# Kernel tuning notes

Hardware: AMD Instinct MI355X
Metric: run time of the kernel (lower is better)

The kernel has to match this reference:

```python
import jax, jax.numpy as jnp
import numpy as np

B, N, C = 1, 2048, 2048
H, KV, D = 32, 8, 64          # query heads, kv heads, head_dim
G = H // KV                    # groups per kv head
EPS = 1e-6
ROPE_BASE = 10000.0


def rmsnorm(x, w, eps=EPS):
    # normalize over the full last dim (H*D or KV*D), as in the module
    var = jnp.mean(jnp.square(x), axis=-1, keepdims=True)
    return x * jax.lax.rsqrt(var + eps) * w


def rope(x):
    # x: [B, N, h, D]; interleaved-pair rotary embedding (torchtune style)
    b, n, h, d = x.shape
    half = d // 2
    inv_freq = 1.0 / (ROPE_BASE ** (jnp.arange(0, d, 2, dtype=jnp.float32) / d))  # [half]
    ang = jnp.arange(n, dtype=jnp.float32)[:, None] * inv_freq[None, :]           # [N, half]
    cos = jnp.cos(ang)[None, :, None, :]
    sin = jnp.sin(ang)[None, :, None, :]
    xr = x.reshape(b, n, h, half, 2)
    x1, x2 = xr[..., 0], xr[..., 1]
    out = jnp.stack([x1 * cos - x2 * sin, x1 * sin + x2 * cos], axis=-1)
    return out.reshape(b, n, h, d)


def setup_inputs() -> dict:
    key = jax.random.key(0)
    ks = jax.random.split(key, 7)
    s = 0.02
    return {
        "x": jax.random.normal(ks[0], (B, N, C), dtype=jnp.float32),
        "wq": jax.random.normal(ks[1], (H * D, C), dtype=jnp.float32) * s,
        "wk": jax.random.normal(ks[2], (KV * D, C), dtype=jnp.float32) * s,
        "wv": jax.random.normal(ks[3], (KV * D, C), dtype=jnp.float32) * s,
        "wo": jax.random.normal(ks[4], (C, C), dtype=jnp.float32) * s,
        "q_norm_w": 1.0 + 0.01 * jax.random.normal(ks[5], (H * D,), dtype=jnp.float32),
        "k_norm_w": 1.0 + 0.01 * jax.random.normal(ks[6], (KV * D,), dtype=jnp.float32),
    }


def reference(x, wq, wk, wv, wo, q_norm_w, k_norm_w):
    scale = D ** -0.5
    q = jnp.einsum("bnc,oc->bno", x, wq)   # [B,N,H*D]
    k = jnp.einsum("bnc,oc->bno", x, wk)   # [B,N,KV*D]
    v = jnp.einsum("bnc,oc->bno", x, wv)
    q = rmsnorm(q, q_norm_w)               # QK-RMSNorm over flat head dims
    k = rmsnorm(k, k_norm_w)
    q = rope(q.reshape(B, N, H, D))
    k = rope(k.reshape(B, N, KV, D))
    v = v.reshape(B, N, KV, D)
    # GQA: group query heads per kv head, no explicit k/v expand
    qg = q.reshape(B, N, KV, G, D)
    scores = jnp.einsum("bnkgd,bmkd->bkgnm", qg, k) * scale  # [B,KV,G,N,N]
    causal = jnp.tril(jnp.ones((N, N), dtype=bool))
    scores = jnp.where(causal[None, None, None], scores, jnp.finfo(scores.dtype).min)
    probs = jax.nn.softmax(scores, axis=-1)
    out = jnp.einsum("bkgnm,bmkd->bnkgd", probs, v).reshape(B, N, H * D)
    return jnp.einsum("bno,co->bnc", out, wo)
```

## Files before the change

### kernel.cpp

```cpp
#include <hip/hip_runtime.h>

typedef __attribute__((ext_vector_type(8))) short short8;
typedef __attribute__((ext_vector_type(4))) float f32x4;

#define MFMA_BF16 __builtin_amdgcn_mfma_f32_16x16x32_bf16

__device__ __forceinline__ unsigned short f2bf(float f) {
  unsigned u = __builtin_bit_cast(unsigned, f);
  u += 0x7fffu + ((u >> 16) & 1u);
  return (unsigned short)(u >> 16);
}

__device__ __forceinline__ unsigned cvtpk(float a, float b) {
  unsigned r;
  asm("v_cvt_pk_bf16_f32 %0, %1, %2" : "=v"(r) : "v"(a), "v"(b));
  return r;
}

__global__ __launch_bounds__(256) void f2b5_kernel(const float* __restrict__ x,
                                                   const float* __restrict__ wq,
                                                   const float* __restrict__ wk,
                                                   const float* __restrict__ wv,
                                                   const float* __restrict__ wo,
                                                   unsigned short* __restrict__ xb,
                                                   unsigned short* __restrict__ wb,
                                                   unsigned short* __restrict__ wob) {
  const int b = blockIdx.x;
  const float* src;
  unsigned short* dst;
  int base;
  if (b < 4096)      { src = x;  dst = xb;                base = b; }
  else if (b < 8192) { src = wq; dst = wb;                base = b - 4096; }
  else if (b < 9216) { src = wk; dst = wb + 2048 * 2048;  base = b - 8192; }
  else if (b < 10240){ src = wv; dst = wb + 2560 * 2048;  base = b - 9216; }
  else               { src = wo; dst = wob;               base = b - 10240; }
  const int i = base * 256 + threadIdx.x;
  const float4 v = ((const float4*)src)[i];
  ushort4 o = make_ushort4(f2bf(v.x), f2bf(v.y), f2bf(v.z), f2bf(v.w));
  ((ushort4*)dst)[i] = o;
}

__global__ __launch_bounds__(256) void trig_kernel(float* __restrict__ cosT, float* __restrict__ sinT) {
  int i = blockIdx.x * 256 + threadIdx.x;
  int n = i >> 5, f = i & 31;
  double ang = (double)n * pow(10000.0, -(double)f / 32.0);
  cosT[i] = (float)cos(ang);
  sinT[i] = (float)sin(ang);
}

__global__ __launch_bounds__(256) void add2_kernel(const float* __restrict__ a,
                                                   const float* __restrict__ b,
                                                   float* __restrict__ o) {
  int i = blockIdx.x * 256 + threadIdx.x;
#pragma unroll
  for (int s = 0; s < 2; ++s) {
    const float4 u = ((const float4*)a)[i], v = ((const float4*)b)[i];
    ((float4*)o)[i] = make_float4(u.x + v.x, u.y + v.y, u.z + v.z, u.w + v.w);
    i += 524288;
  }
}

__global__ __launch_bounds__(256) void gemm_bt(const short* __restrict__ A,
                                               const short* __restrict__ B,
                                               float* __restrict__ C,
                                               int M, int N, int K, int KC) {
  __shared__ __align__(16) short As[2][128 * 32];
  __shared__ __align__(16) short Bs[2][128 * 32];
  const int tid = threadIdx.x;
  const int w = tid >> 6, lane = tid & 63;
  const int fr = lane & 15, fs = lane >> 4;
  const size_t brow = (size_t)blockIdx.y * 128, bcol = (size_t)blockIdx.x * 128;
  const int wr = (w >> 1) * 64, wc = (w & 1) * 64;
  const int lr = tid >> 2;
  const int lcS = ((tid & 3) ^ (lr & 3)) * 8;
  const int ks = blockIdx.z * KC;
  C += (size_t)blockIdx.z * ((size_t)M * N);
  const short* ga = A + (brow + lr) * (size_t)K + lcS + ks;
  const short* gb = B + (bcol + lr) * (size_t)K + lcS + ks;
  f32x4 acc[4][4] = {};

  auto stage = [&](int sb, int k0) {
    short* lA = As[sb] + w * 512;
    short* lB = Bs[sb] + w * 512;
    __builtin_amdgcn_global_load_lds((__attribute__((address_space(1))) void*)(ga + k0),
                                     (__attribute__((address_space(3))) void*)(lA), 16, 0, 0);
    __builtin_amdgcn_global_load_lds((__attribute__((address_space(1))) void*)(ga + (size_t)64 * K + k0),
                                     (__attribute__((address_space(3))) void*)(lA + 2048), 16, 0, 0);
    __builtin_amdgcn_global_load_lds((__attribute__((address_space(1))) void*)(gb + k0),
                                     (__attribute__((address_space(3))) void*)(lB), 16, 0, 0);
    __builtin_amdgcn_global_load_lds((__attribute__((address_space(1))) void*)(gb + (size_t)64 * K + k0),
                                     (__attribute__((address_space(3))) void*)(lB + 2048), 16, 0, 0);
  };

  const int nk = KC >> 5;
  stage(0, 0);
  __syncthreads();
  int buf = 0;
  for (int t = 0; t < nk; ++t) {
    if (t + 1 < nk) stage(buf ^ 1, (t + 1) * 32);
    short8 af[4], bfr[4];
#pragma unroll
    for (int m = 0; m < 4; ++m)
      af[m] = *(const short8*)(As[buf] + (wr + m * 16 + fr) * 32 + ((fs ^ (fr & 3)) * 8));
#pragma unroll
    for (int n = 0; n < 4; ++n)
      bfr[n] = *(const short8*)(Bs[buf] + (wc + n * 16 + fr) * 32 + ((fs ^ (fr & 3)) * 8));
#pragma unroll
    for (int m = 0; m < 4; ++m)
#pragma unroll
      for (int n = 0; n < 4; ++n)
        acc[m][n] = MFMA_BF16(af[m], bfr[n], acc[m][n], 0, 0, 0);
    __syncthreads();
    buf ^= 1;
  }
#pragma unroll
  for (int m = 0; m < 4; ++m)
#pragma unroll
    for (int n = 0; n < 4; ++n)
#pragma unroll
      for (int j = 0; j < 4; ++j)
        C[(brow + wr + m * 16 + fs * 4 + j) * (size_t)N + bcol + wc + n * 16 + fr] = acc[m][n][j];
}

__global__ __launch_bounds__(256) void prep_kernel(const float* __restrict__ qkv,
                                                   const float* __restrict__ qw,
                                                   const float* __restrict__ kw,
                                                   const float* __restrict__ cosT,
                                                   const float* __restrict__ sinT,
                                                   short* __restrict__ qb,
                                                   short* __restrict__ kb,
                                                   short* __restrict__ vbt) {
  const int n = blockIdx.x, t = threadIdx.x;
  const int w = t >> 6, lane = t & 63;
  __shared__ float redq[4], redk[4];
  const float* rowA = qkv + (size_t)n * 3072;
  const float* rowB = rowA + 6291456;
  const float* cT = cosT + n * 32;
  const float* sT = sinT + n * 32;
  const float4* r4a = (const float4*)rowA;
  const float4* r4b = (const float4*)rowB;
  float4 a0 = r4a[t * 2], a1 = r4b[t * 2];
  float4 b0 = r4a[t * 2 + 1], b1 = r4b[t * 2 + 1];
  float4 a = make_float4(a0.x + a1.x, a0.y + a1.y, a0.z + a1.z, a0.w + a1.w);
  float4 b = make_float4(b0.x + b1.x, b0.y + b1.y, b0.z + b1.z, b0.w + b1.w);
  float ss = a.x*a.x + a.y*a.y + a.z*a.z + a.w*a.w + b.x*b.x + b.y*b.y + b.z*b.z + b.w*b.w;
#pragma unroll
  for (int off = 32; off > 0; off >>= 1) ss += __shfl_xor(ss, off);
  if (lane == 0) redq[w] = ss;
  __syncthreads();
  float rsq = rsqrtf((redq[0] + redq[1] + redq[2] + redq[3]) * (1.0f / 2048.f) + 1e-6f)
              * 0.125f * 1.44269504088896f;
  const int base = t * 8;
  float y[8] = {a.x, a.y, a.z, a.w, b.x, b.y, b.z, b.w};
#pragma unroll
  for (int e = 0; e < 8; ++e) y[e] *= rsq * qw[base + e];
  short8 ov;
  const int dbase = base & 63;
#pragma unroll
  for (int p = 0; p < 4; ++p) {
    float c = cT[(dbase >> 1) + p], s = sT[(dbase >> 1) + p];
    float x1 = y[2 * p], x2 = y[2 * p + 1];
    ov[2 * p]     = (short)f2bf(x1 * c - x2 * s);
    ov[2 * p + 1] = (short)f2bf(x1 * s + x2 * c);
  }
  const int h = base >> 6;
  *(short8*)(qb + ((size_t)h * 2048 + n) * 64 + dbase) = ov;
  const int ki = t * 2;
  float2 k0 = *(const float2*)(rowA + 2048 + ki);
  float2 k1 = *(const float2*)(rowB + 2048 + ki);
  float2 kv2 = make_float2(k0.x + k1.x, k0.y + k1.y);
  float ssk = kv2.x * kv2.x + kv2.y * kv2.y;
#pragma unroll
  for (int off = 32; off > 0; off >>= 1) ssk += __shfl_xor(ssk, off);
  if (lane == 0) redk[w] = ssk;
  __syncthreads();
  float rsk = rsqrtf((redk[0] + redk[1] + redk[2] + redk[3]) * (1.0f / 512.f) + 1e-6f);
  float z0 = kv2.x * rsk * kw[ki], z1 = kv2.y * rsk * kw[ki + 1];
  const int kd = ki & 63, kvh = ki >> 6;
  {
    float c = cT[kd >> 1], s = sT[kd >> 1];
    ushort2 o2 = make_ushort2(f2bf(z0 * c - z1 * s), f2bf(z0 * s + z1 * c));
    *(ushort2*)(kb + ((size_t)kvh * 2048 + n) * 64 + kd) = o2;
  }
  float2 v0 = *(const float2*)(rowA + 2560 + ki);
  float2 v1 = *(const float2*)(rowB + 2560 + ki);
  vbt[((size_t)kvh * 64 + kd) * 2048 + n]       = (short)f2bf(v0.x + v1.x);
  vbt[((size_t)kvh * 64 + kd + 1) * 2048 + n]   = (short)f2bf(v0.y + v1.y);
}

__global__ __launch_bounds__(256, 4) void attn_kernel(const short* __restrict__ qb,
                                                      const short* __restrict__ kb,
                                                      const short* __restrict__ vbt,
                                                      short* __restrict__ ab) {
  const int bid = blockIdx.x;
  const int h = bid & 31;
  const int qblk = 31 - (bid >> 5);
  const int kvh = h >> 2;
  const int tid = threadIdx.x;
  const int w = tid >> 6, lane = tid & 63;
  const int fr = lane & 15, fs = lane >> 4;
  const int q0w = qblk * 64 + w * 16;
  const int q_lane = q0w + fr;
  __shared__ __align__(16) short Ks[2][64][64];
  __shared__ __align__(16) short Vs[2][64][64];
  __shared__ __align__(16) short Ps[4][16][64];
  const short* Kb = kb + (size_t)kvh * 2048 * 64;
  const short* Vb = vbt + (size_t)kvh * 64 * 2048;
  short8 qf[2];
  {
    const short* qrow = qb + ((size_t)h * 2048 + q_lane) * 64;
    qf[0] = *(const short8*)(qrow + fs * 8);
    qf[1] = *(const short8*)(qrow + 32 + fs * 8);
  }
  short8 ones8;
#pragma unroll
  for (int e = 0; e < 8; ++e) ones8[e] = (short)0x3F80;
  f32x4 accO[4] = {};
  f32x4 lacc = {};
  float m = -1e30f;
  short* prow = &Ps[w][fr][0];
  const int swz = (fr & 7) << 1;

  const int rS = lane >> 3;
  const int cS = (lane & 7) ^ rS;
  auto stage = [&](int sb, int kv0s) {
#pragma unroll
    for (int i = 0; i < 2; ++i) {
      int r = i * 32 + w * 8 + rS;
      __builtin_amdgcn_global_load_lds(
          (__attribute__((address_space(1))) void*)(Kb + (size_t)(kv0s + r) * 64 + cS * 8),
          (__attribute__((address_space(3))) void*)(&Ks[sb][0][0] + i * 2048 + w * 512), 16, 0, 0);
      __builtin_amdgcn_global_load_lds(
          (__attribute__((address_space(1))) void*)(Vb + (size_t)r * 2048 + kv0s + cS * 8),
          (__attribute__((address_space(3))) void*)(&Vs[sb][0][0] + i * 2048 + w * 512), 16, 0, 0);
    }
  };

  const int ntiles = qblk + 1;
  int buf = 0;
  stage(0, 0);
  __syncthreads();
  for (int t = 0; t < ntiles; ++t) {
    const int kv0 = t * 64;
    if (t + 1 < ntiles) stage(buf ^ 1, (t + 1) * 64);
    const short* KsB = &Ks[buf][0][0];
    const short* VsB = &Vs[buf][0][0];
    const int sw = (fr & 7);
    f32x4 sc[4];
#pragma unroll
    for (int ct = 0; ct < 4; ++ct) {
      const int rk = ct * 16 + fr;
      short8 kf0 = *(const short8*)(KsB + rk * 64 + ((fs ^ sw) * 8));
      short8 kf1 = *(const short8*)(KsB + rk * 64 + (((4 + fs) ^ sw) * 8));
      f32x4 a = {};
      a = MFMA_BF16(kf0, qf[0], a, 0, 0, 0);
      a = MFMA_BF16(kf1, qf[1], a, 0, 0, 0);
      sc[ct] = a;
    }
    if (t == qblk) {
#pragma unroll
      for (int ct = 0; ct < 4; ++ct) {
        const int kvb = kv0 + ct * 16 + fs * 4;
#pragma unroll
        for (int j = 0; j < 4; ++j)
          if (kvb + j > q_lane) sc[ct][j] = -1e30f;
      }
    }
    float v0m = fmaxf(fmaxf(sc[0][0], sc[0][1]), fmaxf(sc[0][2], sc[0][3]));
    float v1m = fmaxf(fmaxf(sc[1][0], sc[1][1]), fmaxf(sc[1][2], sc[1][3]));
    float v2m = fmaxf(fmaxf(sc[2][0], sc[2][1]), fmaxf(sc[2][2], sc[2][3]));
    float v3m = fmaxf(fmaxf(sc[3][0], sc[3][1]), fmaxf(sc[3][2], sc[3][3]));
    float vmax = fmaxf(fmaxf(v0m, v1m), fmaxf(v2m, v3m));
    vmax = fmaxf(vmax, __shfl_xor(vmax, 16));
    vmax = fmaxf(vmax, __shfl_xor(vmax, 32));
    if (!__all(vmax - m <= 8.0f)) {
      float mn = fmaxf(m, vmax);
      float resc = exp2f(m - mn);
      m = mn;
      lacc *= resc;
#pragma unroll
      for (int dt = 0; dt < 4; ++dt)
#pragma unroll
        for (int j = 0; j < 4; ++j) accO[dt][j] *= resc;
    }
#pragma unroll
    for (int ct = 0; ct < 4; ++ct) {
      uint2 pk;
      pk.x = cvtpk(exp2f(sc[ct][0] - m), exp2f(sc[ct][1] - m));
      pk.y = cvtpk(exp2f(sc[ct][2] - m), exp2f(sc[ct][3] - m));
      *(uint2*)(prow + (((ct * 4 + fs) ^ swz) * 4)) = pk;
    }
    short8 pa[2];
#pragma unroll
    for (int s = 0; s < 2; ++s)
      pa[s] = *(const short8*)(prow + (((s * 8 + fs * 2) ^ swz) * 4));
    __builtin_amdgcn_s_setprio(1);
    lacc = MFMA_BF16(ones8, pa[0], lacc, 0, 0, 0);
    lacc = MFMA_BF16(ones8, pa[1], lacc, 0, 0, 0);
#pragma unroll
    for (int dt = 0; dt < 4; ++dt) {
      const int rv = dt * 16 + fr;
      short8 vf0 = *(const short8*)(VsB + rv * 64 + ((fs ^ sw) * 8));
      short8 vf1 = *(const short8*)(VsB + rv * 64 + (((4 + fs) ^ sw) * 8));
      accO[dt] = MFMA_BF16(vf0, pa[0], accO[dt], 0, 0, 0);
      accO[dt] = MFMA_BF16(vf1, pa[1], accO[dt], 0, 0, 0);
    }
    __builtin_amdgcn_s_setprio(0);
    __syncthreads();
    buf ^= 1;
  }
  const float inv = 1.0f / lacc[0];
  short* orow = ab + (size_t)q_lane * 2048 + h * 64;
#pragma unroll
  for (int dt = 0; dt < 4; ++dt) {
    uint2 o;
    o.x = cvtpk(accO[dt][0] * inv, accO[dt][1] * inv);
    o.y = cvtpk(accO[dt][2] * inv, accO[dt][3] * inv);
    *(uint2*)(orow + dt * 16 + fs * 4) = o;
  }
}

extern "C" void kernel_launch(void* const* d_in, const int* in_sizes, int n_in,
                              void* d_out, int out_size, void* d_ws, size_t ws_size,
                              hipStream_t stream) {
  const float* x  = (const float*)d_in[0];
  const float* wq = (const float*)d_in[1];
  const float* wk = (const float*)d_in[2];
  const float* wv = (const float*)d_in[3];
  const float* wo = (const float*)d_in[4];
  const float* qw = (const float*)d_in[5];
  const float* kw = (const float*)d_in[6];
  float* out = (float*)d_out;
  char* ws = (char*)d_ws;
  short* xb    = (short*)(ws + 0);
  short* wb    = (short*)(ws + 8388608);
  short* wob   = (short*)(ws + 20971520);
  float* qkvfA = (float*)(ws + 29360128);
  float* qkvfB = (float*)(ws + 54525952);
  short* qb    = (short*)(ws + 79691776);
  short* kb    = (short*)(ws + 88080384);
  short* vbt   = (short*)(ws + 90177536);
  float* cosT  = (float*)(ws + 92274688);
  float* sinT  = (float*)(ws + 92536832);
  short* ab = xb;
  float* po0 = qkvfA;
  float* po1 = qkvfA + 4194304;
  (void)qkvfB; (void)ws_size;

  f2b5_kernel<<<14336, 256, 0, stream>>>(x, wq, wk, wv, wo,
                                         (unsigned short*)xb, (unsigned short*)wb,
                                         (unsigned short*)wob);
  trig_kernel<<<256, 256, 0, stream>>>(cosT, sinT);
  gemm_bt<<<dim3(24, 16, 2), 256, 0, stream>>>(xb, wb, qkvfA, 2048, 3072, 2048, 1024);
  prep_kernel<<<2048, 256, 0, stream>>>(qkvfA, qw, kw, cosT, sinT, qb, kb, vbt);
  attn_kernel<<<1024, 256, 0, stream>>>(qb, kb, vbt, ab);
  gemm_bt<<<dim3(16, 16, 2), 256, 0, stream>>>(ab, wob, po0, 2048, 2048, 2048, 1024);
  add2_kernel<<<2048, 256, 0, stream>>>(po0, po1, out);
}
```

Baseline: 155.0 us.

## Process 128 query rows per attention block with two 16-row tiles per wave

The attention kernel now gives each wave 32 query rows (two 16-row MFMA tiles), so every block covers 128 queries and the grid halves to 512 blocks. Each K/V tile staged in LDS is reused across twice as many queries, which cuts global-to-LDS traffic and staging overhead per unit of work. Block order is changed to pair heavy and light causal blocks, and waves skip KV tiles that lie entirely above their rows. In exchange, register pressure roughly doubles (occupancy hint drops from 4 to 2), there are fewer blocks to spread over the CUs, and waves inside a block finish their causal work unevenly.

```diff
diff --git a/kernel.cpp b/kernel.cpp
--- a/kernel.cpp
+++ b/kernel.cpp
@@ -188,37 +188,37 @@
   vbt[((size_t)kvh * 64 + kd + 1) * 2048 + n]   = (short)f2bf(v0.y + v1.y);
 }
 
-__global__ __launch_bounds__(256, 4) void attn_kernel(const short* __restrict__ qb,
+__global__ __launch_bounds__(256, 2) void attn_kernel(const short* __restrict__ qb,
                                                       const short* __restrict__ kb,
                                                       const short* __restrict__ vbt,
                                                       short* __restrict__ ab) {
   const int bid = blockIdx.x;
   const int h = bid & 31;
-  const int qblk = 31 - (bid >> 5);
+  const int idx = bid >> 5;
+  const int qblk = idx < 8 ? 15 - idx : idx - 8;
   const int kvh = h >> 2;
   const int tid = threadIdx.x;
   const int w = tid >> 6, lane = tid & 63;
   const int fr = lane & 15, fs = lane >> 4;
-  const int q0w = qblk * 64 + w * 16;
-  const int q_lane = q0w + fr;
+  const int q0w = qblk * 128 + w * 32;
   __shared__ __align__(16) short Ks[2][64][64];
   __shared__ __align__(16) short Vs[2][64][64];
-  __shared__ __align__(16) short Ps[4][16][64];
+  __shared__ __align__(16) short Ps[4][2][16][64];
   const short* Kb = kb + (size_t)kvh * 2048 * 64;
   const short* Vb = vbt + (size_t)kvh * 64 * 2048;
-  short8 qf[2];
-  {
-    const short* qrow = qb + ((size_t)h * 2048 + q_lane) * 64;
-    qf[0] = *(const short8*)(qrow + fs * 8);
-    qf[1] = *(const short8*)(qrow + 32 + fs * 8);
+  short8 qf[2][2];
+#pragma unroll
+  for (int m = 0; m < 2; ++m) {
+    const short* qrow = qb + ((size_t)h * 2048 + q0w + m * 16 + fr) * 64;
+    qf[m][0] = *(const short8*)(qrow + fs * 8);
+    qf[m][1] = *(const short8*)(qrow + 32 + fs * 8);
   }
   short8 ones8;
 #pragma unroll
   for (int e = 0; e < 8; ++e) ones8[e] = (short)0x3F80;
-  f32x4 accO[4] = {};
-  f32x4 lacc = {};
-  float m = -1e30f;
-  short* prow = &Ps[w][fr][0];
+  f32x4 accO[2][4] = {};
+  f32x4 lacc[2] = {};
+  float mrun[2] = {-1e30f, -1e30f};
   const int swz = (fr & 7) << 1;
 
   const int rS = lane >> 3;
@@ -236,87 +236,113 @@
     }
   };
 
-  const int ntiles = qblk + 1;
+  const int ntiles = qblk * 2 + 2;
   int buf = 0;
   stage(0, 0);
   __syncthreads();
   for (int t = 0; t < ntiles; ++t) {
     const int kv0 = t * 64;
     if (t + 1 < ntiles) stage(buf ^ 1, (t + 1) * 64);
-    const short* KsB = &Ks[buf][0][0];
-    const short* VsB = &Vs[buf][0][0];
-    const int sw = (fr & 7);
-    f32x4 sc[4];
-#pragma unroll
-    for (int ct = 0; ct < 4; ++ct) {
-      const int rk = ct * 16 + fr;
-      short8 kf0 = *(const short8*)(KsB + rk * 64 + ((fs ^ sw) * 8));
-      short8 kf1 = *(const short8*)(KsB + rk * 64 + (((4 + fs) ^ sw) * 8));
-      f32x4 a = {};
-      a = MFMA_BF16(kf0, qf[0], a, 0, 0, 0);
-      a = MFMA_BF16(kf1, qf[1], a, 0, 0, 0);
-      sc[ct] = a;
+    if (kv0 <= q0w + 31) {
+      const short* KsB = &Ks[buf][0][0];
+      const short* VsB = &Vs[buf][0][0];
+      const int sw = (fr & 7);
+      f32x4 sc[2][4];
+#pragma unroll
+      for (int ct = 0; ct < 4; ++ct) {
+        const int rk = ct * 16 + fr;
+        short8 kf0 = *(const short8*)(KsB + rk * 64 + ((fs ^ sw) * 8));
+        short8 kf1 = *(const short8*)(KsB + rk * 64 + (((4 + fs) ^ sw) * 8));
+#pragma unroll
+        for (int m = 0; m < 2; ++m) {
+          f32x4 a = {};
+          a = MFMA_BF16(kf0, qf[m][0], a, 0, 0, 0);
+          a = MFMA_BF16(kf1, qf[m][1], a, 0, 0, 0);
+          sc[m][ct] = a;
+        }
+      }
+#pragma unroll
+      for (int m = 0; m < 2; ++m) {
+        const int qm = q0w + m * 16 + fr;
+        if (kv0 + 63 > qm - fr) {
+#pragma unroll
+          for (int ct = 0; ct < 4; ++ct) {
+            const int kvb = kv0 + ct * 16 + fs * 4;
+#pragma unroll
+            for (int j = 0; j < 4; ++j)
+              if (kvb + j > qm) sc[m][ct][j] = -1e30f;
+          }
+        }
+      }
+#pragma unroll
+      for (int m = 0; m < 2; ++m) {
+        float v0m = fmaxf(fmaxf(sc[m][0][0], sc[m][0][1]), fmaxf(sc[m][0][2], sc[m][0][3]));
+        float v1m = fmaxf(fmaxf(sc[m][1][0], sc[m][1][1]), fmaxf(sc[m][1][2], sc[m][1][3]));
+        float v2m = fmaxf(fmaxf(sc[m][2][0], sc[m][2][1]), fmaxf(sc[m][2][2], sc[m][2][3]));
+        float v3m = fmaxf(fmaxf(sc[m][3][0], sc[m][3][1]), fmaxf(sc[m][3][2], sc[m][3][3]));
+        float vmax = fmaxf(fmaxf(v0m, v1m), fmaxf(v2m, v3m));
+        vmax = fmaxf(vmax, __shfl_xor(vmax, 16));
+        vmax = fmaxf(vmax, __shfl_xor(vmax, 32));
+        if (!__all(vmax - mrun[m] <= 8.0f)) {
+          float mn = fmaxf(mrun[m], vmax);
+          float resc = exp2f(mrun[m] - mn);
+          mrun[m] = mn;
+          lacc[m] *= resc;
+#pragma unroll
+          for (int dt = 0; dt < 4; ++dt)
+#pragma unroll
+            for (int j = 0; j < 4; ++j) accO[m][dt][j] *= resc;
+        }
+        short* prow = &Ps[w][m][fr][0];
+#pragma unroll
+        for (int ct = 0; ct < 4; ++ct) {
+          uint2 pk;
+          pk.x = cvtpk(exp2f(sc[m][ct][0] - mrun[m]), exp2f(sc[m][ct][1] - mrun[m]));
+          pk.y = cvtpk(exp2f(sc[m][ct][2] - mrun[m]), exp2f(sc[m][ct][3] - mrun[m]));
+          *(uint2*)(prow + (((ct * 4 + fs) ^ swz) * 4)) = pk;
+        }
+      }
+      short8 pa[2][2];
+#pragma unroll
+      for (int m = 0; m < 2; ++m) {
+        short* prow = &Ps[w][m][fr][0];
+#pragma unroll
+        for (int s = 0; s < 2; ++s)
+          pa[m][s] = *(const short8*)(prow + (((s * 8 + fs * 2) ^ swz) * 4));
+      }
+      __builtin_amdgcn_s_setprio(1);
+#pragma unroll
+      for (int m = 0; m < 2; ++m) {
+        lacc[m] = MFMA_BF16(ones8, pa[m][0], lacc[m], 0, 0, 0);
+        lacc[m] = MFMA_BF16(ones8, pa[m][1], lacc[m], 0, 0, 0);
+      }
+#pragma unroll
+      for (int dt = 0; dt < 4; ++dt) {
+        const int rv = dt * 16 + fr;
+        short8 vf0 = *(const short8*)(VsB + rv * 64 + ((fs ^ sw) * 8));
+        short8 vf1 = *(const short8*)(VsB + rv * 64 + (((4 + fs) ^ sw) * 8));
+#pragma unroll
+        for (int m = 0; m < 2; ++m) {
+          accO[m][dt] = MFMA_BF16(vf0, pa[m][0], accO[m][dt], 0, 0, 0);
+          accO[m][dt] = MFMA_BF16(vf1, pa[m][1], accO[m][dt], 0, 0, 0);
+        }
+      }
+      __builtin_amdgcn_s_setprio(0);
     }
-    if (t == qblk) {
-#pragma unroll
-      for (int ct = 0; ct < 4; ++ct) {
-        const int kvb = kv0 + ct * 16 + fs * 4;
-#pragma unroll
-        for (int j = 0; j < 4; ++j)
-          if (kvb + j > q_lane) sc[ct][j] = -1e30f;
-      }
-    }
-    float v0m = fmaxf(fmaxf(sc[0][0], sc[0][1]), fmaxf(sc[0][2], sc[0][3]));
-    float v1m = fmaxf(fmaxf(sc[1][0], sc[1][1]), fmaxf(sc[1][2], sc[1][3]));
-    float v2m = fmaxf(fmaxf(sc[2][0], sc[2][1]), fmaxf(sc[2][2], sc[2][3]));
-    float v3m = fmaxf(fmaxf(sc[3][0], sc[3][1]), fmaxf(sc[3][2], sc[3][3]));
-    float vmax = fmaxf(fmaxf(v0m, v1m), fmaxf(v2m, v3m));
-    vmax = fmaxf(vmax, __shfl_xor(vmax, 16));
-    vmax = fmaxf(vmax, __shfl_xor(vmax, 32));
-    if (!__all(vmax - m <= 8.0f)) {
-      float mn = fmaxf(m, vmax);
-      float resc = exp2f(m - mn);
-      m = mn;
-      lacc *= resc;
-#pragma unroll
-      for (int dt = 0; dt < 4; ++dt)
-#pragma unroll
-        for (int j = 0; j < 4; ++j) accO[dt][j] *= resc;
-    }
-#pragma unroll
-    for (int ct = 0; ct < 4; ++ct) {
-      uint2 pk;
-      pk.x = cvtpk(exp2f(sc[ct][0] - m), exp2f(sc[ct][1] - m));
-      pk.y = cvtpk(exp2f(sc[ct][2] - m), exp2f(sc[ct][3] - m));
-      *(uint2*)(prow + (((ct * 4 + fs) ^ swz) * 4)) = pk;
-    }
-    short8 pa[2];
-#pragma unroll
-    for (int s = 0; s < 2; ++s)
-      pa[s] = *(const short8*)(prow + (((s * 8 + fs * 2) ^ swz) * 4));
-    __builtin_amdgcn_s_setprio(1);
-    lacc = MFMA_BF16(ones8, pa[0], lacc, 0, 0, 0);
-    lacc = MFMA_BF16(ones8, pa[1], lacc, 0, 0, 0);
-#pragma unroll
-    for (int dt = 0; dt < 4; ++dt) {
-      const int rv = dt * 16 + fr;
-      short8 vf0 = *(const short8*)(VsB + rv * 64 + ((fs ^ sw) * 8));
-      short8 vf1 = *(const short8*)(VsB + rv * 64 + (((4 + fs) ^ sw) * 8));
-      accO[dt] = MFMA_BF16(vf0, pa[0], accO[dt], 0, 0, 0);
-      accO[dt] = MFMA_BF16(vf1, pa[1], accO[dt], 0, 0, 0);
-    }
-    __builtin_amdgcn_s_setprio(0);
     __syncthreads();
     buf ^= 1;
   }
-  const float inv = 1.0f / lacc[0];
-  short* orow = ab + (size_t)q_lane * 2048 + h * 64;
-#pragma unroll
-  for (int dt = 0; dt < 4; ++dt) {
-    uint2 o;
-    o.x = cvtpk(accO[dt][0] * inv, accO[dt][1] * inv);
-    o.y = cvtpk(accO[dt][2] * inv, accO[dt][3] * inv);
-    *(uint2*)(orow + dt * 16 + fs * 4) = o;
+#pragma unroll
+  for (int m = 0; m < 2; ++m) {
+    const float inv = 1.0f / lacc[m][0];
+    short* orow = ab + (size_t)(q0w + m * 16 + fr) * 2048 + h * 64;
+#pragma unroll
+    for (int dt = 0; dt < 4; ++dt) {
+      uint2 o;
+      o.x = cvtpk(accO[m][dt][0] * inv, accO[m][dt][1] * inv);
+      o.y = cvtpk(accO[m][dt][2] * inv, accO[m][dt][3] * inv);
+      *(uint2*)(orow + dt * 16 + fs * 4) = o;
+    }
   }
 }
 
@@ -353,7 +379,7 @@
   trig_kernel<<<256, 256, 0, stream>>>(cosT, sinT);
   gemm_bt<<<dim3(24, 16, 2), 256, 0, stream>>>(xb, wb, qkvfA, 2048, 3072, 2048, 1024);
   prep_kernel<<<2048, 256, 0, stream>>>(qkvfA, qw, kw, cosT, sinT, qb, kb, vbt);
-  attn_kernel<<<1024, 256, 0, stream>>>(qb, kb, vbt, ab);
+  attn_kernel<<<512, 256, 0, stream>>>(qb, kb, vbt, ab);
   gemm_bt<<<dim3(16, 16, 2), 256, 0, stream>>>(ab, wob, po0, 2048, 2048, 2048, 1024);
   add2_kernel<<<2048, 256, 0, stream>>>(po0, po1, out);
 }
```

New measurement: 172.7 us. 11.4% more time.

## Split causal attention KV range in two halves and merge partials

Applied to the files above, without the earlier changes.

Each (head, query block) attention block is split into two blocks that each process half of the causal KV tiles. Each writes an unnormalized bf16 partial output plus its running max and row sum, and a new merge kernel combines the two with rescaling. The goal is to shorten the longest per-block critical path from causal imbalance and to double the available parallelism. The cost is an extra kernel launch, extra partial-output memory traffic, and one more bf16 rounding of unnormalized partials.

```diff
diff --git a/kernel.cpp b/kernel.cpp
--- a/kernel.cpp
+++ b/kernel.cpp
@@ -15,6 +15,10 @@
   unsigned r;
   asm("v_cvt_pk_bf16_f32 %0, %1, %2" : "=v"(r) : "v"(a), "v"(b));
   return r;
+}
+
+__device__ __forceinline__ float b2f(short s) {
+  return __builtin_bit_cast(float, ((unsigned)(unsigned short)s) << 16);
 }
 
 __global__ __launch_bounds__(256) void f2b5_kernel(const float* __restrict__ x,
@@ -191,16 +195,31 @@
 __global__ __launch_bounds__(256, 4) void attn_kernel(const short* __restrict__ qb,
                                                       const short* __restrict__ kb,
                                                       const short* __restrict__ vbt,
-                                                      short* __restrict__ ab) {
+                                                      short* __restrict__ opart,
+                                                      float2* __restrict__ mlb) {
   const int bid = blockIdx.x;
   const int h = bid & 31;
-  const int qblk = 31 - (bid >> 5);
+  const int idx = bid >> 5;
+  const int qblk = 31 - (idx >> 1);
+  const int half = idx & 1;
   const int kvh = h >> 2;
   const int tid = threadIdx.x;
   const int w = tid >> 6, lane = tid & 63;
   const int fr = lane & 15, fs = lane >> 4;
   const int q0w = qblk * 64 + w * 16;
   const int q_lane = q0w + fr;
+  const int nt = qblk + 1;
+  const int nh0 = (nt + 1) >> 1;
+  const int tbeg = half ? nh0 : 0;
+  const int tend = half ? nt : nh0;
+  short* orow = opart + (size_t)half * 4194304 + ((size_t)h * 2048 + q_lane) * 64;
+  if (tbeg >= tend) {
+    uint2 z = make_uint2(0u, 0u);
+#pragma unroll
+    for (int dt = 0; dt < 4; ++dt) *(uint2*)(orow + dt * 16 + fs * 4) = z;
+    if (lane < 16) mlb[half * 65536 + h * 2048 + q_lane] = make_float2(-1e30f, 0.f);
+    return;
+  }
   __shared__ __align__(16) short Ks[2][64][64];
   __shared__ __align__(16) short Vs[2][64][64];
   __shared__ __align__(16) short Ps[4][16][64];
@@ -236,13 +255,12 @@
     }
   };
 
-  const int ntiles = qblk + 1;
   int buf = 0;
-  stage(0, 0);
+  stage(0, tbeg * 64);
   __syncthreads();
-  for (int t = 0; t < ntiles; ++t) {
+  for (int t = tbeg; t < tend; ++t) {
     const int kv0 = t * 64;
-    if (t + 1 < ntiles) stage(buf ^ 1, (t + 1) * 64);
+    if (t + 1 < tend) stage(buf ^ 1, (t + 1) * 64);
     const short* KsB = &Ks[buf][0][0];
     const short* VsB = &Vs[buf][0][0];
     const int sw = (fr & 7);
@@ -309,15 +327,36 @@
     __syncthreads();
     buf ^= 1;
   }
-  const float inv = 1.0f / lacc[0];
-  short* orow = ab + (size_t)q_lane * 2048 + h * 64;
 #pragma unroll
   for (int dt = 0; dt < 4; ++dt) {
     uint2 o;
-    o.x = cvtpk(accO[dt][0] * inv, accO[dt][1] * inv);
-    o.y = cvtpk(accO[dt][2] * inv, accO[dt][3] * inv);
+    o.x = cvtpk(accO[dt][0], accO[dt][1]);
+    o.y = cvtpk(accO[dt][2], accO[dt][3]);
     *(uint2*)(orow + dt * 16 + fs * 4) = o;
   }
+  if (lane < 16) mlb[half * 65536 + h * 2048 + q_lane] = make_float2(m, lacc[0]);
+}
+
+__global__ __launch_bounds__(256) void merge_kernel(const short* __restrict__ opart,
+                                                    const float2* __restrict__ mlb,
+                                                    short* __restrict__ ab) {
+  const int gid = blockIdx.x * 256 + threadIdx.x;
+  const int dc = gid & 7;
+  const int q = (gid >> 3) & 2047;
+  const int h = gid >> 14;
+  const int hq = h * 2048 + q;
+  const float2 ml0 = mlb[hq], ml1 = mlb[65536 + hq];
+  const float mm = fmaxf(ml0.x, ml1.x);
+  const float s0 = exp2f(ml0.x - mm), s1 = exp2f(ml1.x - mm);
+  const float inv = 1.0f / (ml0.y * s0 + ml1.y * s1);
+  const size_t b0 = (size_t)hq * 64 + dc * 8;
+  const short8 o0 = *(const short8*)(opart + b0);
+  const short8 o1 = *(const short8*)(opart + b0 + 4194304);
+  short8 o;
+#pragma unroll
+  for (int j = 0; j < 8; ++j)
+    o[j] = (short)f2bf((b2f(o0[j]) * s0 + b2f(o1[j]) * s1) * inv);
+  *(short8*)(ab + (size_t)q * 2048 + h * 64 + dc * 8) = o;
 }
 
 extern "C" void kernel_launch(void* const* d_in, const int* in_sizes, int n_in,
@@ -345,6 +384,8 @@
   short* ab = xb;
   float* po0 = qkvfA;
   float* po1 = qkvfA + 4194304;
+  short* opart = (short*)(ws + 62914560);
+  float2* mlb  = (float2*)(ws + 8388608);
   (void)qkvfB; (void)ws_size;
 
   f2b5_kernel<<<14336, 256, 0, stream>>>(x, wq, wk, wv, wo,
@@ -353,7 +394,8 @@
   trig_kernel<<<256, 256, 0, stream>>>(cosT, sinT);
   gemm_bt<<<dim3(24, 16, 2), 256, 0, stream>>>(xb, wb, qkvfA, 2048, 3072, 2048, 1024);
   prep_kernel<<<2048, 256, 0, stream>>>(qkvfA, qw, kw, cosT, sinT, qb, kb, vbt);
-  attn_kernel<<<1024, 256, 0, stream>>>(qb, kb, vbt, ab);
+  attn_kernel<<<2048, 256, 0, stream>>>(qb, kb, vbt, opart, mlb);
+  merge_kernel<<<2048, 256, 0, stream>>>(opart, mlb, ab);
   gemm_bt<<<dim3(16, 16, 2), 256, 0, stream>>>(ab, wob, po0, 2048, 2048, 2048, 1024);
   add2_kernel<<<2048, 256, 0, stream>>>(po0, po1, out);
 }
```

New measurement: 156.0 us. Within noise of the previous version (+0.7%).
